# Optimization experiments

Hardware: AMD Instinct MI355X
Metric: run time of the kernel (lower is better)

## Reference

```python
import jax, jax.numpy as jnp
import numpy as np

B, S, DM, H = 16, 4096, 512, 4
HD = DM // H  # head_dim = 128
EPS = 1e-5


def setup_inputs() -> dict:
    key = jax.random.key(0)
    ks = jax.random.split(key, 9)
    sc = 1.0 / np.sqrt(DM)
    inp = {
        "x": jax.random.normal(ks[0], (B, S, DM), dtype=jnp.float32),
        "Wq_w": jax.random.normal(ks[1], (DM, DM), dtype=jnp.float32) * sc,
        "Wq_b": jnp.zeros((DM,), dtype=jnp.float32),
        "Wk_w": jax.random.normal(ks[2], (DM, DM), dtype=jnp.float32) * sc,
        "Wk_b": jnp.zeros((DM,), dtype=jnp.float32),
        "Wv_w": jax.random.normal(ks[3], (DM, DM), dtype=jnp.float32) * sc,
        "Wv_b": jnp.zeros((DM,), dtype=jnp.float32),
        "Wo_w": jax.random.normal(ks[4], (DM, DM), dtype=jnp.float32) * sc,
        "Wo_b": jnp.zeros((DM,), dtype=jnp.float32),
        "ln_g": jnp.ones((DM,), dtype=jnp.float32),
        "ln_b": jnp.zeros((DM,), dtype=jnp.float32),
    }
    return inp


def _forward(x, Wq_w, Wq_b, Wk_w, Wk_b, Wv_w, Wv_b, Wo_w, Wo_b, ln_g, ln_b):
    b, s, _ = x.shape
    # Linear projections, viewed as [B,S,H,HD] exactly as the torch code does
    Q = (x @ Wq_w.T + Wq_b).reshape(b, s, H, HD)
    K = (x @ Wk_w.T + Wk_b).reshape(b, s, H, HD)
    V = (x @ Wv_w.T + Wv_b).reshape(b, s, H, HD)
    # NOTE: source never permutes heads to dim 1, so attention is over the
    # HEAD axis per token: scores [B,S,H,H]
    scores = jnp.einsum("bshd,bstd->bsht", Q, K) / np.sqrt(HD).astype(np.float32)
    attn = jax.nn.softmax(scores, axis=-1)  # dropout is identity in eval
    out = jnp.einsum("bsht,bstd->bshd", attn, V).reshape(b, s, DM)
    out = out @ Wo_w.T + Wo_b
    y = out + x  # input_dim == output_dim -> residual branch taken
    mu = jnp.mean(y, axis=-1, keepdims=True)
    var = jnp.mean((y - mu) ** 2, axis=-1, keepdims=True)
    return (y - mu) * jax.lax.rsqrt(var + EPS) * ln_g + ln_b


def reference(x, Wq_w, Wq_b, Wk_w, Wk_b, Wv_w, Wv_b, Wo_w, Wo_b, ln_g, ln_b):
    return _forward(x, Wq_w, Wq_b, Wk_w, Wk_b, Wv_w, Wv_b, Wo_w, Wo_b, ln_g, ln_b)
```

## Files before the change

kernel.cpp:

```cpp
#include <hip/hip_runtime.h>
#include <stdint.h>

#define NTOK 65536
#define DMODEL 512
#define QKVN 1536
#define LN_EPS 1e-5f

typedef __attribute__((ext_vector_type(8))) short short8;
typedef __attribute__((ext_vector_type(8))) unsigned short ushort8;
typedef __attribute__((ext_vector_type(4))) float float4_t;
typedef __attribute__((ext_vector_type(4))) unsigned int uint4_t;

static __device__ __forceinline__ float bf2f(unsigned short u) {
    union { unsigned int i; float f; } c; c.i = ((unsigned int)u) << 16; return c.f;
}
static __device__ __forceinline__ unsigned short f2bf(float f) {
    union { float f; unsigned int i; } c; c.f = f;
    unsigned int x = c.i;
    return (unsigned short)((x + 0x7fffu + ((x >> 16) & 1u)) >> 16);
}
static __device__ __forceinline__ unsigned int cvt_pk_bf16(float lo, float hi) {
    unsigned int r;
    asm("v_cvt_pk_bf16_f32 %0, %1, %2" : "=v"(r) : "v"(lo), "v"(hi));
    return r;
}
static __device__ __forceinline__ void gload_lds16(const void* g, void* l) {
    __builtin_amdgcn_global_load_lds((const __attribute__((address_space(1))) void*)g,
                                     (__attribute__((address_space(3))) void*)l, 16, 0, 0);
}

#define BAR() __builtin_amdgcn_s_barrier()
#define WAITL0() asm volatile("s_waitcnt lgkmcnt(0)" ::: "memory")
#define WVM(n) asm volatile("s_waitcnt vmcnt(" #n ")" ::: "memory")
#define MFMA(a, b, c) __builtin_amdgcn_mfma_f32_16x16x32_bf16((a), (b), (c), 0, 0, 0)

__global__ __launch_bounds__(256) void cast_x_kernel(const float* __restrict__ x,
                                                     unsigned short* __restrict__ xb, int n8) {
    int stride = gridDim.x * blockDim.x;
    for (int i = blockIdx.x * blockDim.x + threadIdx.x; i < n8; i += stride) {
        const float4_t* p = (const float4_t*)(x + (size_t)i * 8);
        float4_t a = p[0], b = p[1];
        ushort8 v;
        v[0] = f2bf(a[0]); v[1] = f2bf(a[1]); v[2] = f2bf(a[2]); v[3] = f2bf(a[3]);
        v[4] = f2bf(b[0]); v[5] = f2bf(b[1]); v[6] = f2bf(b[2]); v[7] = f2bf(b[3]);
        *(ushort8*)(xb + (size_t)i * 8) = v;
    }
}

__global__ __launch_bounds__(256) void prep_w_kernel(
    const float* __restrict__ wq, const float* __restrict__ wk, const float* __restrict__ wv,
    const float* __restrict__ wo,
    const float* __restrict__ bq, const float* __restrict__ bk, const float* __restrict__ bv,
    unsigned short* __restrict__ wqkv, unsigned short* __restrict__ wpack,
    float* __restrict__ bias_qkv) {
    const int WN = DMODEL * DMODEL;
    int tid = blockIdx.x * blockDim.x + threadIdx.x;
    int stride = gridDim.x * blockDim.x;
    for (int j = tid; j < 3 * WN; j += stride) {
        int seg = j / WN, idx = j - seg * WN;
        const float* src = (seg == 0) ? wq : (seg == 1) ? wk : wv;
        wqkv[j] = f2bf(src[idx]);
    }
    for (int j = tid; j < WN; j += stride) {
        int e = j & 7, l = (j >> 3) & 63, nf = (j >> 9) & 31, kt = j >> 14;
        int row = nf * 16 + (l & 15);
        int k = kt * 32 + ((l >> 4) << 3) + e;
        wpack[j] = f2bf(wo[row * 512 + k]);
    }
    for (int j = tid; j < QKVN; j += stride)
        bias_qkv[j] = (j < 512) ? bq[j] : (j < 1024) ? bk[j - 512] : bv[j - 1024];
}

__global__ __launch_bounds__(512, 2) void gemm1_kernel(
    const unsigned short* __restrict__ A, const unsigned short* __restrict__ Bw,
    const float* __restrict__ bias, unsigned short* __restrict__ Cout) {
    __shared__ unsigned short As[4][256 * 32];
    __shared__ unsigned short Bs[4][256 * 32];

    const int b = blockIdx.x;
    const int L = (b & 7) * 192 + (b >> 3);
    const int bm = L / 6;
    const int bn = L - bm * 6;

    const int t = threadIdx.x;
    const int lane = t & 63;
    const int w = t >> 6;
    const int wm = w >> 2, wn = w & 3;

    const unsigned short* Ab = A + (size_t)bm * 256 * 512;
    const unsigned short* Bb = Bw + (size_t)bn * 256 * 512;

    const int i0 = t, i1 = 512 + t;
    const int r0 = i0 >> 2, s0 = (i0 & 3) ^ ((r0 >> 1) & 3);
    const int r1 = i1 >> 2, s1 = (i1 & 3) ^ ((r1 >> 1) & 3);

#define STAGE_A1(kt) do { \
        gload_lds16(Ab + r0 * 512 + (kt) * 32 + s0 * 8, &As[(kt) & 3][i0 * 8]); \
        gload_lds16(Ab + r1 * 512 + (kt) * 32 + s1 * 8, &As[(kt) & 3][i1 * 8]); } while (0)
#define STAGE_B1(kt) do { \
        gload_lds16(Bb + r0 * 512 + (kt) * 32 + s0 * 8, &Bs[(kt) & 3][i0 * 8]); \
        gload_lds16(Bb + r1 * 512 + (kt) * 32 + s1 * 8, &Bs[(kt) & 3][i1 * 8]); } while (0)

    int aoff[8], boff[4];
#pragma unroll
    for (int m = 0; m < 8; m++) {
        int row = wm * 128 + m * 16 + (lane & 15);
        aoff[m] = row * 32 + (((lane >> 4) ^ ((row >> 1) & 3)) * 8);
    }
#pragma unroll
    for (int n = 0; n < 4; n++) {
        int row = wn * 64 + n * 16 + (lane & 15);
        boff[n] = row * 32 + (((lane >> 4) ^ ((row >> 1) & 3)) * 8);
    }

    float4_t acc[8][4];
#pragma unroll
    for (int m = 0; m < 8; m++)
#pragma unroll
        for (int n = 0; n < 4; n++) acc[m][n] = (float4_t){0.f, 0.f, 0.f, 0.f};

    STAGE_A1(0); STAGE_B1(0);
    STAGE_A1(1); STAGE_B1(1);
    STAGE_A1(2); STAGE_B1(2);
    WVM(8);
    BAR();

    short8 ar[8], br[4];
#pragma unroll
    for (int kt = 0; kt < 16; ++kt) {
        const int sl = kt & 3;
#pragma unroll
        for (int m = 0; m < 8; m++) ar[m] = *(const short8*)&As[sl][aoff[m]];
        br[0] = *(const short8*)&Bs[sl][boff[0]];
        br[1] = *(const short8*)&Bs[sl][boff[1]];
        if (kt <= 12) STAGE_A1(kt + 3);
        BAR();
        WAITL0();
        __builtin_amdgcn_s_setprio(1);
#pragma unroll
        for (int m = 0; m < 8; m++) {
            acc[m][0] = MFMA(ar[m], br[0], acc[m][0]);
            acc[m][1] = MFMA(ar[m], br[1], acc[m][1]);
        }
        __builtin_amdgcn_s_setprio(0);
        BAR();
        br[2] = *(const short8*)&Bs[sl][boff[2]];
        br[3] = *(const short8*)&Bs[sl][boff[3]];
        if (kt <= 12) STAGE_B1(kt + 3);
        BAR();
        WAITL0();
        __builtin_amdgcn_s_setprio(1);
#pragma unroll
        for (int m = 0; m < 8; m++) {
            acc[m][2] = MFMA(ar[m], br[2], acc[m][2]);
            acc[m][3] = MFMA(ar[m], br[3], acc[m][3]);
        }
        __builtin_amdgcn_s_setprio(0);
        if (kt <= 12) { WVM(8); }
        else if (kt == 13) { WVM(4); }
        else if (kt == 14) { WVM(0); }
        BAR();
    }

    const int orow0 = bm * 256 + wm * 128;
    const int ocol0 = bn * 256 + wn * 64;
#pragma unroll
    for (int m = 0; m < 8; m++) {
#pragma unroll
        for (int n = 0; n < 4; n++) {
            int col = ocol0 + n * 16 + (lane & 15);
            float bv = bias[col];
#pragma unroll
            for (int j = 0; j < 4; j++) {
                int row = orow0 + m * 16 + (lane >> 4) * 4 + j;
                Cout[(size_t)row * QKVN + col] = f2bf(acc[m][n][j] + bv);
            }
        }
    }
#undef STAGE_A1
#undef STAGE_B1
}

__global__ __launch_bounds__(256, 4) void attn_o_ln_kernel(
    const unsigned short* __restrict__ qkv, const unsigned short* __restrict__ Wpack,
    const float* __restrict__ bo, const float* __restrict__ xres,
    const float* __restrict__ lng, const float* __restrict__ lnb,
    float* __restrict__ Y) {
    __shared__ __align__(16) unsigned char AOs[16 * 1024];
    float* red = (float*)AOs;

    const int T0 = blockIdx.x * 16;
    const int t = threadIdx.x;
    const int lane = t & 63;
    const int w = t >> 6;
    const int g = lane >> 4;
    const int sl = lane & 15;

    const float scale = 0.08838834764831845f;

    {
        const int tr = w * 4 + g;
        const unsigned short* base = qkv + (size_t)(T0 + tr) * QKVN + sl * 8;

        short8 qr[4], kr[4], vr[4];
#pragma unroll
        for (int h = 0; h < 4; h++) {
            qr[h] = *(const short8*)(base + h * 128);
            kr[h] = *(const short8*)(base + 512 + h * 128);
            vr[h] = *(const short8*)(base + 1024 + h * 128);
        }
#pragma unroll
        for (int h = 0; h < 4; h++) {
            float qf[8];
#pragma unroll
            for (int d = 0; d < 8; d++) qf[d] = bf2f((unsigned short)qr[h][d]);
            float s[4];
#pragma unroll
            for (int tt = 0; tt < 4; tt++) {
                float a0 = 0.f;
#pragma unroll
                for (int d = 0; d < 8; d++) a0 += qf[d] * bf2f((unsigned short)kr[tt][d]);
                s[tt] = a0;
            }
#pragma unroll
            for (int mask = 1; mask < 16; mask <<= 1)
#pragma unroll
                for (int tt = 0; tt < 4; tt++)
                    s[tt] += __shfl_xor(s[tt], mask, 64);
            float m0 = fmaxf(fmaxf(s[0], s[1]), fmaxf(s[2], s[3])) * scale;
            float p[4];
            float sum = 0.f;
#pragma unroll
            for (int tt = 0; tt < 4; tt++) { p[tt] = __expf(s[tt] * scale - m0); sum += p[tt]; }
            float rr = __frcp_rn(sum);
            float o[8];
#pragma unroll
            for (int d = 0; d < 8; d++) o[d] = 0.f;
#pragma unroll
            for (int tt = 0; tt < 4; tt++) {
                float ph = p[tt] * rr;
#pragma unroll
                for (int d = 0; d < 8; d++) o[d] += ph * bf2f((unsigned short)vr[tt][d]);
            }
            uint4_t pk;
            pk[0] = cvt_pk_bf16(o[0], o[1]);
            pk[1] = cvt_pk_bf16(o[2], o[3]);
            pk[2] = cvt_pk_bf16(o[4], o[5]);
            pk[3] = cvt_pk_bf16(o[6], o[7]);
            int off = tr * 1024 + ((h * 256 + sl * 16) ^ ((tr & 7) << 4));
            *(uint4_t*)(AOs + off) = pk;
        }
    }
    __syncthreads();

    const unsigned short* Bb2 = Wpack + ((size_t)(w * 8) * 64 + lane) * 8;
    const int arow = sl;
    const int aswz = (arow & 7) << 4;

    float4_t acc[8];
#pragma unroll
    for (int n = 0; n < 8; n++) acc[n] = (float4_t){0.f, 0.f, 0.f, 0.f};

    short8 bA[8], bB[8];
#pragma unroll
    for (int n = 0; n < 8; n++) bA[n] = *(const short8*)(Bb2 + n * 512);
#pragma unroll
    for (int n = 0; n < 8; n++) bB[n] = *(const short8*)(Bb2 + 16384 + n * 512);

#pragma unroll 1
    for (int kt = 0; kt < 16; kt += 2) {
        short8 a0 = *(const short8*)(AOs + arow * 1024 + ((kt * 64 + g * 16) ^ aswz));
#pragma unroll
        for (int n = 0; n < 8; n++) acc[n] = MFMA(a0, bA[n], acc[n]);
        if (kt + 2 < 16) {
#pragma unroll
            for (int n = 0; n < 8; n++)
                bA[n] = *(const short8*)(Bb2 + (size_t)(kt + 2) * 16384 + n * 512);
        }
        short8 a1 = *(const short8*)(AOs + arow * 1024 + (((kt + 1) * 64 + g * 16) ^ aswz));
#pragma unroll
        for (int n = 0; n < 8; n++) acc[n] = MFMA(a1, bB[n], acc[n]);
        if (kt + 3 < 16) {
#pragma unroll
            for (int n = 0; n < 8; n++)
                bB[n] = *(const short8*)(Bb2 + (size_t)(kt + 3) * 16384 + n * 512);
        }
    }
    __syncthreads();

    float bias8[8], gc8[8], bc8[8];
#pragma unroll
    for (int n = 0; n < 8; n++) {
        int c = w * 128 + n * 16 + sl;
        bias8[n] = bo[c]; gc8[n] = lng[c]; bc8[n] = lnb[c];
    }
#pragma unroll
    for (int j = 0; j < 4; j++) {
        int grow = T0 + g * 4 + j;
        const float* xr = xres + (size_t)grow * 512;
#pragma unroll
        for (int n = 0; n < 8; n++)
            acc[n][j] += bias8[n] + xr[w * 128 + n * 16 + sl];
    }
#pragma unroll
    for (int j = 0; j < 4; j++) {
        float s = 0.f, s2 = 0.f;
#pragma unroll
        for (int n = 0; n < 8; n++) { float v = acc[n][j]; s += v; s2 += v * v; }
#pragma unroll
        for (int mask = 1; mask < 16; mask <<= 1) {
            s += __shfl_xor(s, mask, 64);
            s2 += __shfl_xor(s2, mask, 64);
        }
        if (sl == 0) {
            int rl = g * 4 + j;
            red[(rl * 4 + w) * 2 + 0] = s;
            red[(rl * 4 + w) * 2 + 1] = s2;
        }
    }
    __syncthreads();
#pragma unroll
    for (int j = 0; j < 4; j++) {
        int rl = g * 4 + j;
        float s = 0.f, s2 = 0.f;
#pragma unroll
        for (int i = 0; i < 4; i++) {
            s += red[(rl * 4 + i) * 2 + 0];
            s2 += red[(rl * 4 + i) * 2 + 1];
        }
        float mu = s * (1.f / 512.f);
        float var = s2 * (1.f / 512.f) - mu * mu;
        float inv = rsqrtf(var + LN_EPS);
        float* yp = Y + (size_t)(T0 + rl) * 512;
#pragma unroll
        for (int n = 0; n < 8; n++) {
            int c = w * 128 + n * 16 + sl;
            yp[c] = (acc[n][j] - mu) * inv * gc8[n] + bc8[n];
        }
    }
}

extern "C" void kernel_launch(void* const* d_in, const int* in_sizes, int n_in,
                              void* d_out, int out_size, void* d_ws, size_t ws_size,
                              hipStream_t stream) {
    const float* x   = (const float*)d_in[0];
    const float* wq  = (const float*)d_in[1];
    const float* bq  = (const float*)d_in[2];
    const float* wk  = (const float*)d_in[3];
    const float* bk  = (const float*)d_in[4];
    const float* wv  = (const float*)d_in[5];
    const float* bv  = (const float*)d_in[6];
    const float* wo  = (const float*)d_in[7];
    const float* bo  = (const float*)d_in[8];
    const float* lng = (const float*)d_in[9];
    const float* lnb = (const float*)d_in[10];

    char* ws = (char*)d_ws;
    unsigned short* Xb    = (unsigned short*)(ws);
    unsigned short* Wqkv  = (unsigned short*)(ws + 67108864);
    unsigned short* Wpack = (unsigned short*)(ws + 68681728);
    float*          Bqkv  = (float*)        (ws + 69206016);
    unsigned short* QKV   = (unsigned short*)(ws + 69212160);
    float* Y = (float*)d_out;

    cast_x_kernel<<<2048, 256, 0, stream>>>(x, Xb, NTOK * 512 / 8);
    prep_w_kernel<<<1024, 256, 0, stream>>>(wq, wk, wv, wo, bq, bk, bv, Wqkv, Wpack, Bqkv);

    gemm1_kernel<<<(NTOK / 256) * (QKVN / 256), 512, 0, stream>>>(Xb, Wqkv, Bqkv, QKV);

    attn_o_ln_kernel<<<NTOK / 16, 256, 0, stream>>>(QKV, Wpack, bo, x, lng, lnb, Y);
}
```

Baseline: 323.3 us.

## Fuse fp32-to-bf16 cast of x into QKV GEMM operand staging

Drops the separate cast kernel that read x in fp32 and wrote a bf16 copy to workspace. The QKV GEMM now stages fp32 tiles of x into LDS and converts them to bf16 with v_cvt_pk_bf16 while building MFMA operands. The LDS pipeline shrinks from four stages to three, A tiles take twice the LDS space, and the k-loop is no longer unrolled. This removes a full pass over x plus the bf16 copy, but the GEMM now reads twice as many A bytes, repeated across the six column blocks. Occupancy and latency hiding may also drop.

```diff
diff --git a/kernel.cpp b/kernel.cpp
--- a/kernel.cpp
+++ b/kernel.cpp
@@ -33,19 +33,6 @@
 #define WAITL0() asm volatile("s_waitcnt lgkmcnt(0)" ::: "memory")
 #define WVM(n) asm volatile("s_waitcnt vmcnt(" #n ")" ::: "memory")
 #define MFMA(a, b, c) __builtin_amdgcn_mfma_f32_16x16x32_bf16((a), (b), (c), 0, 0, 0)
-
-__global__ __launch_bounds__(256) void cast_x_kernel(const float* __restrict__ x,
-                                                     unsigned short* __restrict__ xb, int n8) {
-    int stride = gridDim.x * blockDim.x;
-    for (int i = blockIdx.x * blockDim.x + threadIdx.x; i < n8; i += stride) {
-        const float4_t* p = (const float4_t*)(x + (size_t)i * 8);
-        float4_t a = p[0], b = p[1];
-        ushort8 v;
-        v[0] = f2bf(a[0]); v[1] = f2bf(a[1]); v[2] = f2bf(a[2]); v[3] = f2bf(a[3]);
-        v[4] = f2bf(b[0]); v[5] = f2bf(b[1]); v[6] = f2bf(b[2]); v[7] = f2bf(b[3]);
-        *(ushort8*)(xb + (size_t)i * 8) = v;
-    }
-}
 
 __global__ __launch_bounds__(256) void prep_w_kernel(
     const float* __restrict__ wq, const float* __restrict__ wk, const float* __restrict__ wv,
@@ -72,10 +59,10 @@
 }
 
 __global__ __launch_bounds__(512, 2) void gemm1_kernel(
-    const unsigned short* __restrict__ A, const unsigned short* __restrict__ Bw,
+    const float* __restrict__ X, const unsigned short* __restrict__ Bw,
     const float* __restrict__ bias, unsigned short* __restrict__ Cout) {
-    __shared__ unsigned short As[4][256 * 32];
-    __shared__ unsigned short Bs[4][256 * 32];
+    __shared__ float As[3][8192];
+    __shared__ unsigned short Bs[3][8192];
 
     const int b = blockIdx.x;
     const int L = (b & 7) * 192 + (b >> 3);
@@ -86,31 +73,38 @@
     const int lane = t & 63;
     const int w = t >> 6;
     const int wm = w >> 2, wn = w & 3;
-
-    const unsigned short* Ab = A + (size_t)bm * 256 * 512;
+    const int kg = lane >> 4;
+
+    const float* Af = X + (size_t)bm * 256 * 512;
     const unsigned short* Bb = Bw + (size_t)bn * 256 * 512;
 
+#define STAGE_A1(kt) do { _Pragma("unroll") \
+        for (int c = 0; c < 4; c++) { \
+            int idx = c * 512 + t; \
+            int row = idx >> 3; \
+            int s = (idx & 7) ^ (row & 7); \
+            gload_lds16(Af + (size_t)row * 512 + (kt) * 32 + s * 4, \
+                        (char*)As[(kt) % 3] + idx * 16); \
+        } } while (0)
     const int i0 = t, i1 = 512 + t;
     const int r0 = i0 >> 2, s0 = (i0 & 3) ^ ((r0 >> 1) & 3);
     const int r1 = i1 >> 2, s1 = (i1 & 3) ^ ((r1 >> 1) & 3);
-
-#define STAGE_A1(kt) do { \
-        gload_lds16(Ab + r0 * 512 + (kt) * 32 + s0 * 8, &As[(kt) & 3][i0 * 8]); \
-        gload_lds16(Ab + r1 * 512 + (kt) * 32 + s1 * 8, &As[(kt) & 3][i1 * 8]); } while (0)
 #define STAGE_B1(kt) do { \
-        gload_lds16(Bb + r0 * 512 + (kt) * 32 + s0 * 8, &Bs[(kt) & 3][i0 * 8]); \
-        gload_lds16(Bb + r1 * 512 + (kt) * 32 + s1 * 8, &Bs[(kt) & 3][i1 * 8]); } while (0)
-
-    int aoff[8], boff[4];
+        gload_lds16(Bb + r0 * 512 + (kt) * 32 + s0 * 8, &Bs[(kt) % 3][i0 * 8]); \
+        gload_lds16(Bb + r1 * 512 + (kt) * 32 + s1 * 8, &Bs[(kt) % 3][i1 * 8]); } while (0)
+
+    int aoff0[8], aoff1[8];
 #pragma unroll
     for (int m = 0; m < 8; m++) {
         int row = wm * 128 + m * 16 + (lane & 15);
-        aoff[m] = row * 32 + (((lane >> 4) ^ ((row >> 1) & 3)) * 8);
-    }
+        aoff0[m] = row * 8 + ((2 * kg) ^ (row & 7));
+        aoff1[m] = row * 8 + ((2 * kg + 1) ^ (row & 7));
+    }
+    int boff[4];
 #pragma unroll
     for (int n = 0; n < 4; n++) {
         int row = wn * 64 + n * 16 + (lane & 15);
-        boff[n] = row * 32 + (((lane >> 4) ^ ((row >> 1) & 3)) * 8);
+        boff[n] = row * 32 + ((kg ^ ((row >> 1) & 3)) * 8);
     }
 
     float4_t acc[8][4];
@@ -121,19 +115,29 @@
 
     STAGE_A1(0); STAGE_B1(0);
     STAGE_A1(1); STAGE_B1(1);
-    STAGE_A1(2); STAGE_B1(2);
-    WVM(8);
+    WVM(6);
     BAR();
 
+    union CV { uint4_t u; short8 s; };
     short8 ar[8], br[4];
-#pragma unroll
+#pragma unroll 1
     for (int kt = 0; kt < 16; ++kt) {
-        const int sl = kt & 3;
-#pragma unroll
-        for (int m = 0; m < 8; m++) ar[m] = *(const short8*)&As[sl][aoff[m]];
+        const int sl = kt % 3;
+        const float4_t* Ap = (const float4_t*)As[sl];
+#pragma unroll
+        for (int m = 0; m < 8; m++) {
+            float4_t f0 = Ap[aoff0[m]];
+            float4_t f1 = Ap[aoff1[m]];
+            CV cv;
+            cv.u[0] = cvt_pk_bf16(f0[0], f0[1]);
+            cv.u[1] = cvt_pk_bf16(f0[2], f0[3]);
+            cv.u[2] = cvt_pk_bf16(f1[0], f1[1]);
+            cv.u[3] = cvt_pk_bf16(f1[2], f1[3]);
+            ar[m] = cv.s;
+        }
         br[0] = *(const short8*)&Bs[sl][boff[0]];
         br[1] = *(const short8*)&Bs[sl][boff[1]];
-        if (kt <= 12) STAGE_A1(kt + 3);
+        if (kt <= 13) STAGE_A1(kt + 2);
         BAR();
         WAITL0();
         __builtin_amdgcn_s_setprio(1);
@@ -146,7 +150,7 @@
         BAR();
         br[2] = *(const short8*)&Bs[sl][boff[2]];
         br[3] = *(const short8*)&Bs[sl][boff[3]];
-        if (kt <= 12) STAGE_B1(kt + 3);
+        if (kt <= 13) STAGE_B1(kt + 2);
         BAR();
         WAITL0();
         __builtin_amdgcn_s_setprio(1);
@@ -156,8 +160,7 @@
             acc[m][3] = MFMA(ar[m], br[3], acc[m][3]);
         }
         __builtin_amdgcn_s_setprio(0);
-        if (kt <= 12) { WVM(8); }
-        else if (kt == 13) { WVM(4); }
+        if (kt <= 13) { WVM(6); }
         else if (kt == 14) { WVM(0); }
         BAR();
     }
@@ -172,7 +175,7 @@
             float bv = bias[col];
 #pragma unroll
             for (int j = 0; j < 4; j++) {
-                int row = orow0 + m * 16 + (lane >> 4) * 4 + j;
+                int row = orow0 + m * 16 + kg * 4 + j;
                 Cout[(size_t)row * QKVN + col] = f2bf(acc[m][n][j] + bv);
             }
         }
@@ -356,17 +359,15 @@
     const float* lnb = (const float*)d_in[10];
 
     char* ws = (char*)d_ws;
-    unsigned short* Xb    = (unsigned short*)(ws);
-    unsigned short* Wqkv  = (unsigned short*)(ws + 67108864);
-    unsigned short* Wpack = (unsigned short*)(ws + 68681728);
-    float*          Bqkv  = (float*)        (ws + 69206016);
-    unsigned short* QKV   = (unsigned short*)(ws + 69212160);
+    unsigned short* Wqkv  = (unsigned short*)(ws);
+    unsigned short* Wpack = (unsigned short*)(ws + 1572864);
+    float*          Bqkv  = (float*)        (ws + 2097152);
+    unsigned short* QKV   = (unsigned short*)(ws + 2103296);
     float* Y = (float*)d_out;
 
-    cast_x_kernel<<<2048, 256, 0, stream>>>(x, Xb, NTOK * 512 / 8);
     prep_w_kernel<<<1024, 256, 0, stream>>>(wq, wk, wv, wo, bq, bk, bv, Wqkv, Wpack, Bqkv);
 
-    gemm1_kernel<<<(NTOK / 256) * (QKVN / 256), 512, 0, stream>>>(Xb, Wqkv, Bqkv, QKV);
+    gemm1_kernel<<<(NTOK / 256) * (QKVN / 256), 512, 0, stream>>>(x, Wqkv, Bqkv, QKV);
 
     attn_o_ln_kernel<<<NTOK / 16, 256, 0, stream>>>(QKV, Wpack, bo, x, lng, lnb, Y);
 }
```

Result: slower. 330.0 us (+2.1%).
